# Kernel optimization log

Measured on AMD Instinct MI355X. Metric: run time of the kernel, lower is better.

## Reference

```python
import jax, jax.numpy as jnp
import numpy as np

B, T, D, H = 4096, 128, 32, 64

def _gru_layer(x, W_ih, W_hh, b_ih, b_hh):
    # x: [B, T, in]; W_ih: [3H, in]; W_hh: [3H, H]
    xg = jnp.einsum('bti,gi->btg', x, W_ih) + b_ih  # [B, T, 3H] input gates, one big GEMM
    def step(h, xg_t):
        gh = h @ W_hh.T + b_hh                      # [B, 3H]
        xr, xz, xn = jnp.split(xg_t, 3, axis=-1)
        hr, hz, hn = jnp.split(gh, 3, axis=-1)
        r = jax.nn.sigmoid(xr + hr)
        z = jax.nn.sigmoid(xz + hz)
        n = jnp.tanh(xn + r * hn)
        h_new = (1.0 - z) * n + z * h
        return h_new, h_new
    h0 = jnp.zeros((x.shape[0], W_hh.shape[1]), x.dtype)
    _, hs = jax.lax.scan(step, h0, jnp.swapaxes(xg, 0, 1))  # scan over time
    return jnp.swapaxes(hs, 0, 1)                   # [B, T, H]

def setup_inputs() -> dict:
    key = jax.random.key(0)
    ks = jax.random.split(key, 12)
    s = 0.1
    return {
        'x':     jax.random.normal(ks[0], (B, T, D), jnp.float32),
        'W_ih0': jax.random.normal(ks[1], (3 * H, D), jnp.float32) * s,
        'W_hh0': jax.random.normal(ks[2], (3 * H, H), jnp.float32) * s,
        'b_ih0': jax.random.normal(ks[3], (3 * H,), jnp.float32) * s,
        'b_hh0': jax.random.normal(ks[4], (3 * H,), jnp.float32) * s,
        'W_ih1': jax.random.normal(ks[5], (3 * H, H), jnp.float32) * s,
        'W_hh1': jax.random.normal(ks[6], (3 * H, H), jnp.float32) * s,
        'b_ih1': jax.random.normal(ks[7], (3 * H,), jnp.float32) * s,
        'b_hh1': jax.random.normal(ks[8], (3 * H,), jnp.float32) * s,
        'fc_w':  jax.random.normal(ks[9], (1, H), jnp.float32) * s,
        'fc_b':  jax.random.normal(ks[10], (1,), jnp.float32) * s,
    }

def reference(x, W_ih0, W_hh0, b_ih0, b_hh0, W_ih1, W_hh1, b_ih1, b_hh1, fc_w, fc_b):
    h1 = _gru_layer(x, W_ih0, W_hh0, b_ih0, b_hh0)   # layer 0
    h2 = _gru_layer(h1, W_ih1, W_hh1, b_ih1, b_hh1)  # layer 1
    last = h2[:, -1, :]                              # [B, H]
    out = last @ fc_w.T + fc_b                       # [B, 1]
    return jnp.squeeze(out, axis=-1)                 # [B]
```

## Files before the change

kernel.cpp:

```cpp
#include <hip/hip_runtime.h>

typedef _Float16 f16;
typedef f16 f16x8 __attribute__((ext_vector_type(8)));
typedef f16 f16x4 __attribute__((ext_vector_type(4)));
typedef __fp16 h16x2 __attribute__((ext_vector_type(2)));
typedef float f32x4 __attribute__((ext_vector_type(4)));

#define MFMA16(A, B, C) __builtin_amdgcn_mfma_f32_16x16x32_f16((A), (B), (C), 0, 0, 0)

#define LDS_BARRIER() asm volatile("s_waitcnt lgkmcnt(0)\n\ts_barrier" ::: "memory")

__device__ __forceinline__ f16x8 cvt8(float4 a, float4 b) {
  union { h16x2 h[4]; f16x8 v; } u;
  u.h[0] = __builtin_amdgcn_cvt_pkrtz(a.x, a.y);
  u.h[1] = __builtin_amdgcn_cvt_pkrtz(a.z, a.w);
  u.h[2] = __builtin_amdgcn_cvt_pkrtz(b.x, b.y);
  u.h[3] = __builtin_amdgcn_cvt_pkrtz(b.z, b.w);
  return u.v;
}

__device__ __forceinline__ void gates4(const f32x4& aR, const f32x4& aZ,
                                       const f32x4& aXN, const f32x4& aHN,
                                       float hs[4]) {
#pragma unroll
  for (int r = 0; r < 4; ++r) {
    const float ea = __expf(-aR[r]);
    const float eb = __expf(-aZ[r]);
    const float pa = 1.0f + ea, pb = 1.0f + eb;
    const float inv = __builtin_amdgcn_rcpf(pa * pb);
    const float rg = pb * inv;
    const float zg = pa * inv;
    const float y = aXN[r] + rg * aHN[r];
    const float c = __expf(-2.0f * y);
    const float ng = (1.0f - c) * __builtin_amdgcn_rcpf(1.0f + c);
    hs[r] = ng + zg * (hs[r] - ng);
  }
}

__launch_bounds__(512, 2)
__global__ void gru_fused(const float* __restrict__ x,
                          const float* __restrict__ Wih0, const float* __restrict__ Whh0,
                          const float* __restrict__ bih0, const float* __restrict__ bhh0,
                          const float* __restrict__ Wih1, const float* __restrict__ Whh1,
                          const float* __restrict__ bih1, const float* __restrict__ bhh1,
                          const float* __restrict__ fcw, const float* __restrict__ fcb,
                          float* __restrict__ out) {
  __shared__ f16 H0[2][1024];
  __shared__ f16 H1[2][1024];
  __shared__ float red[4][16];

  const int tid = threadIdx.x;
  const int wave = tid >> 6;
  const int lane = tid & 63;
  const int l15 = lane & 15;
  const int q = lane >> 4;
  const int wa = wave & 3;
  const bool isB = wave >= 4;
  const int b0 = blockIdx.x * 16;

  for (int i = tid; i < 2048; i += 512) {
    ((f16*)H0)[i] = (f16)0.0f;
    ((f16*)H1)[i] = (f16)0.0f;
  }

  f16x8 wAx[3];
  f16x8 wAh[3][2];
  f16x8 wBx[3][2];
  f16x8 wBh[3][2];
  f32x4 bR, bZ, bXN, bHN;
  float fw[4] = {0.f, 0.f, 0.f, 0.f};

  if (!isB) {
#pragma unroll
    for (int g = 0; g < 3; ++g) {
      const int row = g * 64 + 16 * wa + l15;
      const float* p = Wih0 + row * 32 + q * 8;
      wAx[g] = cvt8(*(const float4*)p, *(const float4*)(p + 4));
#pragma unroll
      for (int kf = 0; kf < 2; ++kf) {
        const float* ph = Whh0 + row * 64 + kf * 32 + q * 8;
        wAh[g][kf] = cvt8(*(const float4*)ph, *(const float4*)(ph + 4));
      }
    }
#pragma unroll
    for (int r = 0; r < 4; ++r) {
      const int o = 16 * wa + 4 * q + r;
      bR[r] = bih0[o] + bhh0[o];
      bZ[r] = bih0[64 + o] + bhh0[64 + o];
      bXN[r] = bih0[128 + o];
      bHN[r] = bhh0[128 + o];
    }
  } else {
#pragma unroll
    for (int g = 0; g < 3; ++g) {
      const int row = g * 64 + 16 * wa + l15;
#pragma unroll
      for (int kf = 0; kf < 2; ++kf) {
        const float* p1 = Wih1 + row * 64 + kf * 32 + q * 8;
        wBx[g][kf] = cvt8(*(const float4*)p1, *(const float4*)(p1 + 4));
        const float* p2 = Whh1 + row * 64 + kf * 32 + q * 8;
        wBh[g][kf] = cvt8(*(const float4*)p2, *(const float4*)(p2 + 4));
      }
    }
#pragma unroll
    for (int r = 0; r < 4; ++r) {
      const int o = 16 * wa + 4 * q + r;
      bR[r] = bih1[o] + bhh1[o];
      bZ[r] = bih1[64 + o] + bhh1[64 + o];
      bXN[r] = bih1[128 + o];
      bHN[r] = bhh1[128 + o];
      fw[r] = fcw[o];
    }
  }
  const float fcb0 = fcb[0];

  float hs[4] = {0.f, 0.f, 0.f, 0.f};

  const int wk0 = 16 * wa + 4 * q;
  const int widx = ((wk0 >> 3) * 16 + l15) * 8 + (wk0 & 7);

  auto stepA = [&](const f16* H0r, f16* H0w, float4 xav, float4 xbv) {
    const f16x8 xf = cvt8(xav, xbv);
    const f16x8 h0f0 = *(const f16x8*)&H0r[lane * 8];
    const f16x8 h0f1 = *(const f16x8*)&H0r[512 + lane * 8];
    f32x4 aR = bR, aZ = bZ, aXN = bXN, aHN = bHN;
    aR = MFMA16(wAx[0], xf, aR);
    aZ = MFMA16(wAx[1], xf, aZ);
    aXN = MFMA16(wAx[2], xf, aXN);
    aR = MFMA16(wAh[0][0], h0f0, aR);
    aZ = MFMA16(wAh[1][0], h0f0, aZ);
    aHN = MFMA16(wAh[2][0], h0f0, aHN);
    aR = MFMA16(wAh[0][1], h0f1, aR);
    aZ = MFMA16(wAh[1][1], h0f1, aZ);
    aHN = MFMA16(wAh[2][1], h0f1, aHN);
    gates4(aR, aZ, aXN, aHN, hs);
    union { h16x2 h2[2]; f16x4 v; } uw;
    uw.h2[0] = __builtin_amdgcn_cvt_pkrtz(hs[0], hs[1]);
    uw.h2[1] = __builtin_amdgcn_cvt_pkrtz(hs[2], hs[3]);
    *(f16x4*)&H0w[widx] = uw.v;
  };

  auto stepB = [&](const f16* H0r, const f16* H1r, f16* H1w) {
    const f16x8 g0 = *(const f16x8*)&H0r[lane * 8];
    const f16x8 g1 = *(const f16x8*)&H0r[512 + lane * 8];
    const f16x8 h1f0 = *(const f16x8*)&H1r[lane * 8];
    const f16x8 h1f1 = *(const f16x8*)&H1r[512 + lane * 8];
    f32x4 aR = bR, aZ = bZ, aXN = bXN, aHN = bHN;
    aR = MFMA16(wBx[0][0], g0, aR);
    aZ = MFMA16(wBx[1][0], g0, aZ);
    aXN = MFMA16(wBx[2][0], g0, aXN);
    aR = MFMA16(wBx[0][1], g1, aR);
    aZ = MFMA16(wBx[1][1], g1, aZ);
    aXN = MFMA16(wBx[2][1], g1, aXN);
    aR = MFMA16(wBh[0][0], h1f0, aR);
    aZ = MFMA16(wBh[1][0], h1f0, aZ);
    aHN = MFMA16(wBh[2][0], h1f0, aHN);
    aR = MFMA16(wBh[0][1], h1f1, aR);
    aZ = MFMA16(wBh[1][1], h1f1, aZ);
    aHN = MFMA16(wBh[2][1], h1f1, aHN);
    gates4(aR, aZ, aXN, aHN, hs);
    union { h16x2 h2[2]; f16x4 v; } uw;
    uw.h2[0] = __builtin_amdgcn_cvt_pkrtz(hs[0], hs[1]);
    uw.h2[1] = __builtin_amdgcn_cvt_pkrtz(hs[2], hs[3]);
    *(f16x4*)&H1w[widx] = uw.v;
  };

  __syncthreads();

  const float* xbase = x + (size_t)(b0 + l15) * 4096 + q * 8;
  float4 xa0, xb0, xa1, xb1;
  if (!isB) {
    xa0 = *(const float4*)xbase;
    xb0 = *(const float4*)(xbase + 4);
    xa1 = *(const float4*)(xbase + 32);
    xb1 = *(const float4*)(xbase + 36);
  }

  for (int t = 0; t < 128; t += 2) {
    if (!isB) {
      const float4 cxa = xa0, cxb = xb0;
      if (t + 2 < 128) {
        const float* xp = xbase + (t + 2) * 32;
        xa0 = *(const float4*)xp;
        xb0 = *(const float4*)(xp + 4);
      }
      stepA(H0[0], H0[1], cxa, cxb);
    } else if (t > 0) {
      stepB(H0[0], H1[0], H1[1]);
    }
    LDS_BARRIER();

    if (!isB) {
      const float4 cxa = xa1, cxb = xb1;
      if (t + 3 < 128) {
        const float* xp = xbase + (t + 3) * 32;
        xa1 = *(const float4*)xp;
        xb1 = *(const float4*)(xp + 4);
      }
      stepA(H0[1], H0[0], cxa, cxb);
    } else {
      stepB(H0[1], H1[1], H1[0]);
    }
    LDS_BARRIER();
  }
  if (isB) stepB(H0[0], H1[0], H1[1]);

  if (isB) {
    float partial = fw[0] * hs[0] + fw[1] * hs[1] + fw[2] * hs[2] + fw[3] * hs[3];
    partial += __shfl_down(partial, 16, 64);
    partial += __shfl_down(partial, 32, 64);
    if (lane < 16) red[wa][l15] = partial;
  }
  __syncthreads();
  if (tid < 16) out[b0 + tid] = red[0][tid] + red[1][tid] + red[2][tid] + red[3][tid] + fcb0;
}

extern "C" void kernel_launch(void* const* d_in, const int* in_sizes, int n_in,
                              void* d_out, int out_size, void* d_ws, size_t ws_size,
                              hipStream_t stream) {
  (void)in_sizes; (void)n_in; (void)out_size; (void)d_ws; (void)ws_size;
  const float* x    = (const float*)d_in[0];
  const float* Wih0 = (const float*)d_in[1];
  const float* Whh0 = (const float*)d_in[2];
  const float* bih0 = (const float*)d_in[3];
  const float* bhh0 = (const float*)d_in[4];
  const float* Wih1 = (const float*)d_in[5];
  const float* Whh1 = (const float*)d_in[6];
  const float* bih1 = (const float*)d_in[7];
  const float* bhh1 = (const float*)d_in[8];
  const float* fcw  = (const float*)d_in[9];
  const float* fcb  = (const float*)d_in[10];
  float* out = (float*)d_out;

  gru_fused<<<256, 512, 0, stream>>>(x, Wih0, Whh0, bih0, bhh0,
                                     Wih1, Whh1, bih1, bhh1, fcw, fcb, out);
}
```

Measured before the change: 182.5 us.

## Replace block barriers with LDS flag counters between layer waves

Replaces the per-step block-wide barrier with per-layer LDS counters. Waves spin on the counters and increment them atomically, so layer-0 and layer-1 waves can run up to a few steps apart. H0 becomes a four-deep ring buffer, x is prefetched four steps ahead, and the gate math moves to exp2 in packed pairs with MFMA issue reordered. The aim is to stop the two layers serialising on every barrier. The cost is LDS spin-polling traffic and atomics, and correctness relies on the volatile spin loops plus the LGKM drain.

```diff
diff --git a/kernel.cpp b/kernel.cpp
--- a/kernel.cpp
+++ b/kernel.cpp
@@ -5,10 +5,19 @@
 typedef f16 f16x4 __attribute__((ext_vector_type(4)));
 typedef __fp16 h16x2 __attribute__((ext_vector_type(2)));
 typedef float f32x4 __attribute__((ext_vector_type(4)));
+typedef float f32x2 __attribute__((ext_vector_type(2)));
 
 #define MFMA16(A, B, C) __builtin_amdgcn_mfma_f32_16x16x32_f16((A), (B), (C), 0, 0, 0)
 
-#define LDS_BARRIER() asm volatile("s_waitcnt lgkmcnt(0)\n\ts_barrier" ::: "memory")
+#define LGKM_DRAIN() asm volatile("s_waitcnt lgkmcnt(0)" ::: "memory")
+
+__device__ __forceinline__ float E2(float x) {
+#if __has_builtin(__builtin_amdgcn_exp2f)
+  return __builtin_amdgcn_exp2f(x);
+#else
+  return __expf(x * 0.69314718056f);
+#endif
+}
 
 __device__ __forceinline__ f16x8 cvt8(float4 a, float4 b) {
   union { h16x2 h[4]; f16x8 v; } u;
@@ -19,22 +28,37 @@
   return u.v;
 }
 
-__device__ __forceinline__ void gates4(const f32x4& aR, const f32x4& aZ,
-                                       const f32x4& aXN, const f32x4& aHN,
-                                       float hs[4]) {
-#pragma unroll
-  for (int r = 0; r < 4; ++r) {
-    const float ea = __expf(-aR[r]);
-    const float eb = __expf(-aZ[r]);
-    const float pa = 1.0f + ea, pb = 1.0f + eb;
-    const float inv = __builtin_amdgcn_rcpf(pa * pb);
-    const float rg = pb * inv;
-    const float zg = pa * inv;
-    const float y = aXN[r] + rg * aHN[r];
-    const float c = __expf(-2.0f * y);
-    const float ng = (1.0f - c) * __builtin_amdgcn_rcpf(1.0f + c);
-    hs[r] = ng + zg * (hs[r] - ng);
-  }
+__device__ __forceinline__ void wait2(volatile int* fl, int thrA, int thrB) {
+  while (fl[0] < thrA || fl[1] < thrB) { }
+}
+
+__device__ __forceinline__ void gates_pair(f32x2 aR, f32x2 aZ, f32x2 aXN,
+                                           f32x2 aHN, f32x2& hs) {
+  const float K = -1.44269504f;
+  f32x2 mR = aR * K;
+  f32x2 mZ = aZ * K;
+  f32x2 ea, eb;
+  ea[0] = E2(mR[0]); ea[1] = E2(mR[1]);
+  eb[0] = E2(mZ[0]); eb[1] = E2(mZ[1]);
+  f32x2 pa = ea + 1.0f;
+  f32x2 pb = eb + 1.0f;
+  f32x2 prod = pa * pb;
+  f32x2 inv;
+  inv[0] = __builtin_amdgcn_rcpf(prod[0]);
+  inv[1] = __builtin_amdgcn_rcpf(prod[1]);
+  f32x2 rg = pb * inv;
+  f32x2 zg = pa * inv;
+  f32x2 y = rg * aHN + aXN;
+  f32x2 my = y * (2.0f * K);
+  f32x2 c;
+  c[0] = E2(my[0]); c[1] = E2(my[1]);
+  f32x2 num = 1.0f - c;
+  f32x2 den = 1.0f + c;
+  f32x2 rin;
+  rin[0] = __builtin_amdgcn_rcpf(den[0]);
+  rin[1] = __builtin_amdgcn_rcpf(den[1]);
+  f32x2 ng = num * rin;
+  hs = zg * (hs - ng) + ng;
 }
 
 __launch_bounds__(512, 2)
@@ -45,9 +69,10 @@
                           const float* __restrict__ bih1, const float* __restrict__ bhh1,
                           const float* __restrict__ fcw, const float* __restrict__ fcb,
                           float* __restrict__ out) {
-  __shared__ f16 H0[2][1024];
+  __shared__ f16 H0[4][1024];
   __shared__ f16 H1[2][1024];
   __shared__ float red[4][16];
+  __shared__ int flags[2];
 
   const int tid = threadIdx.x;
   const int wave = tid >> 6;
@@ -58,10 +83,9 @@
   const bool isB = wave >= 4;
   const int b0 = blockIdx.x * 16;
 
-  for (int i = tid; i < 2048; i += 512) {
-    ((f16*)H0)[i] = (f16)0.0f;
-    ((f16*)H1)[i] = (f16)0.0f;
-  }
+  for (int i = tid; i < 4096; i += 512) ((f16*)H0)[i] = (f16)0.0f;
+  for (int i = tid; i < 2048; i += 512) ((f16*)H1)[i] = (f16)0.0f;
+  if (tid == 0) { flags[0] = 0; flags[1] = 0; }
 
   f16x8 wAx[3];
   f16x8 wAh[3][2];
@@ -114,103 +138,105 @@
   }
   const float fcb0 = fcb[0];
 
-  float hs[4] = {0.f, 0.f, 0.f, 0.f};
+  f32x2 hsA = {0.f, 0.f}, hsB2 = {0.f, 0.f};
 
   const int wk0 = 16 * wa + 4 * q;
   const int widx = ((wk0 >> 3) * 16 + l15) * 8 + (wk0 & 7);
 
-  auto stepA = [&](const f16* H0r, f16* H0w, float4 xav, float4 xbv) {
-    const f16x8 xf = cvt8(xav, xbv);
-    const f16x8 h0f0 = *(const f16x8*)&H0r[lane * 8];
-    const f16x8 h0f1 = *(const f16x8*)&H0r[512 + lane * 8];
-    f32x4 aR = bR, aZ = bZ, aXN = bXN, aHN = bHN;
-    aR = MFMA16(wAx[0], xf, aR);
-    aZ = MFMA16(wAx[1], xf, aZ);
-    aXN = MFMA16(wAx[2], xf, aXN);
-    aR = MFMA16(wAh[0][0], h0f0, aR);
-    aZ = MFMA16(wAh[1][0], h0f0, aZ);
-    aHN = MFMA16(wAh[2][0], h0f0, aHN);
-    aR = MFMA16(wAh[0][1], h0f1, aR);
-    aZ = MFMA16(wAh[1][1], h0f1, aZ);
-    aHN = MFMA16(wAh[2][1], h0f1, aHN);
-    gates4(aR, aZ, aXN, aHN, hs);
-    union { h16x2 h2[2]; f16x4 v; } uw;
-    uw.h2[0] = __builtin_amdgcn_cvt_pkrtz(hs[0], hs[1]);
-    uw.h2[1] = __builtin_amdgcn_cvt_pkrtz(hs[2], hs[3]);
-    *(f16x4*)&H0w[widx] = uw.v;
-  };
-
-  auto stepB = [&](const f16* H0r, const f16* H1r, f16* H1w) {
-    const f16x8 g0 = *(const f16x8*)&H0r[lane * 8];
-    const f16x8 g1 = *(const f16x8*)&H0r[512 + lane * 8];
-    const f16x8 h1f0 = *(const f16x8*)&H1r[lane * 8];
-    const f16x8 h1f1 = *(const f16x8*)&H1r[512 + lane * 8];
-    f32x4 aR = bR, aZ = bZ, aXN = bXN, aHN = bHN;
-    aR = MFMA16(wBx[0][0], g0, aR);
-    aZ = MFMA16(wBx[1][0], g0, aZ);
-    aXN = MFMA16(wBx[2][0], g0, aXN);
-    aR = MFMA16(wBx[0][1], g1, aR);
-    aZ = MFMA16(wBx[1][1], g1, aZ);
-    aXN = MFMA16(wBx[2][1], g1, aXN);
-    aR = MFMA16(wBh[0][0], h1f0, aR);
-    aZ = MFMA16(wBh[1][0], h1f0, aZ);
-    aHN = MFMA16(wBh[2][0], h1f0, aHN);
-    aR = MFMA16(wBh[0][1], h1f1, aR);
-    aZ = MFMA16(wBh[1][1], h1f1, aZ);
-    aHN = MFMA16(wBh[2][1], h1f1, aHN);
-    gates4(aR, aZ, aXN, aHN, hs);
-    union { h16x2 h2[2]; f16x4 v; } uw;
-    uw.h2[0] = __builtin_amdgcn_cvt_pkrtz(hs[0], hs[1]);
-    uw.h2[1] = __builtin_amdgcn_cvt_pkrtz(hs[2], hs[3]);
-    *(f16x4*)&H1w[widx] = uw.v;
-  };
-
   __syncthreads();
 
-  const float* xbase = x + (size_t)(b0 + l15) * 4096 + q * 8;
-  float4 xa0, xb0, xa1, xb1;
   if (!isB) {
-    xa0 = *(const float4*)xbase;
-    xb0 = *(const float4*)(xbase + 4);
-    xa1 = *(const float4*)(xbase + 32);
-    xb1 = *(const float4*)(xbase + 36);
-  }
-
-  for (int t = 0; t < 128; t += 2) {
-    if (!isB) {
-      const float4 cxa = xa0, cxb = xb0;
-      if (t + 2 < 128) {
-        const float* xp = xbase + (t + 2) * 32;
-        xa0 = *(const float4*)xp;
-        xb0 = *(const float4*)(xp + 4);
+    const float* xbase = x + (size_t)(b0 + l15) * 4096 + q * 8;
+    float4 xa0 = *(const float4*)(xbase +  0), xb0 = *(const float4*)(xbase +  4);
+    float4 xa1 = *(const float4*)(xbase + 32), xb1 = *(const float4*)(xbase + 36);
+    float4 xa2 = *(const float4*)(xbase + 64), xb2 = *(const float4*)(xbase + 68);
+    float4 xa3 = *(const float4*)(xbase + 96), xb3 = *(const float4*)(xbase + 100);
+
+    auto stepA = [&](int t, const f16* H0r, f16* H0w, float4& pxa, float4& pxb) {
+      wait2(flags, 4 * t, 4 * t - 12);
+      const f16x8 xf = cvt8(pxa, pxb);
+      if (t + 4 < 128) {
+        const float* xp = xbase + (t + 4) * 32;
+        pxa = *(const float4*)xp;
+        pxb = *(const float4*)(xp + 4);
       }
-      stepA(H0[0], H0[1], cxa, cxb);
-    } else if (t > 0) {
-      stepB(H0[0], H1[0], H1[1]);
-    }
-    LDS_BARRIER();
-
-    if (!isB) {
-      const float4 cxa = xa1, cxb = xb1;
-      if (t + 3 < 128) {
-        const float* xp = xbase + (t + 3) * 32;
-        xa1 = *(const float4*)xp;
-        xb1 = *(const float4*)(xp + 4);
-      }
-      stepA(H0[1], H0[0], cxa, cxb);
-    } else {
-      stepB(H0[1], H1[1], H1[0]);
-    }
-    LDS_BARRIER();
-  }
-  if (isB) stepB(H0[0], H1[0], H1[1]);
-
-  if (isB) {
-    float partial = fw[0] * hs[0] + fw[1] * hs[1] + fw[2] * hs[2] + fw[3] * hs[3];
+      const f16x8 h0f0 = *(const f16x8*)&H0r[lane * 8];
+      const f16x8 h0f1 = *(const f16x8*)&H0r[512 + lane * 8];
+      f32x4 aR = bR, aZ = bZ, aXN = bXN, aHN = bHN;
+      aR = MFMA16(wAx[0], xf, aR);
+      aZ = MFMA16(wAx[1], xf, aZ);
+      aR = MFMA16(wAh[0][0], h0f0, aR);
+      aZ = MFMA16(wAh[1][0], h0f0, aZ);
+      aR = MFMA16(wAh[0][1], h0f1, aR);
+      aZ = MFMA16(wAh[1][1], h0f1, aZ);
+      aXN = MFMA16(wAx[2], xf, aXN);
+      aHN = MFMA16(wAh[2][0], h0f0, aHN);
+      aHN = MFMA16(wAh[2][1], h0f1, aHN);
+      gates_pair(f32x2{aR[0], aR[1]}, f32x2{aZ[0], aZ[1]},
+                 f32x2{aXN[0], aXN[1]}, f32x2{aHN[0], aHN[1]}, hsA);
+      gates_pair(f32x2{aR[2], aR[3]}, f32x2{aZ[2], aZ[3]},
+                 f32x2{aXN[2], aXN[3]}, f32x2{aHN[2], aHN[3]}, hsB2);
+      union { h16x2 h2[2]; f16x4 v; } uw;
+      uw.h2[0] = __builtin_amdgcn_cvt_pkrtz(hsA[0], hsA[1]);
+      uw.h2[1] = __builtin_amdgcn_cvt_pkrtz(hsB2[0], hsB2[1]);
+      *(f16x4*)&H0w[widx] = uw.v;
+      LGKM_DRAIN();
+      if (lane == 0) atomicAdd(&flags[0], 1);
+    };
+
+#pragma unroll 1
+    for (int t = 0; t < 128; t += 4) {
+      stepA(t,     &H0[3][0], &H0[0][0], xa0, xb0);
+      stepA(t + 1, &H0[0][0], &H0[1][0], xa1, xb1);
+      stepA(t + 2, &H0[1][0], &H0[2][0], xa2, xb2);
+      stepA(t + 3, &H0[2][0], &H0[3][0], xa3, xb3);
+    }
+  } else {
+    auto stepB = [&](int t, const f16* H0r, const f16* H1r, f16* H1w) {
+      wait2(flags, 4 * t + 4, 4 * t);
+      const f16x8 g0 = *(const f16x8*)&H0r[lane * 8];
+      const f16x8 g1 = *(const f16x8*)&H0r[512 + lane * 8];
+      const f16x8 h1f0 = *(const f16x8*)&H1r[lane * 8];
+      const f16x8 h1f1 = *(const f16x8*)&H1r[512 + lane * 8];
+      f32x4 aR = bR, aZ = bZ, aXN = bXN, aHN = bHN;
+      aR = MFMA16(wBx[0][0], g0, aR);
+      aZ = MFMA16(wBx[1][0], g0, aZ);
+      aR = MFMA16(wBx[0][1], g1, aR);
+      aZ = MFMA16(wBx[1][1], g1, aZ);
+      aR = MFMA16(wBh[0][0], h1f0, aR);
+      aZ = MFMA16(wBh[1][0], h1f0, aZ);
+      aR = MFMA16(wBh[0][1], h1f1, aR);
+      aZ = MFMA16(wBh[1][1], h1f1, aZ);
+      aXN = MFMA16(wBx[2][0], g0, aXN);
+      aXN = MFMA16(wBx[2][1], g1, aXN);
+      aHN = MFMA16(wBh[2][0], h1f0, aHN);
+      aHN = MFMA16(wBh[2][1], h1f1, aHN);
+      gates_pair(f32x2{aR[0], aR[1]}, f32x2{aZ[0], aZ[1]},
+                 f32x2{aXN[0], aXN[1]}, f32x2{aHN[0], aHN[1]}, hsA);
+      gates_pair(f32x2{aR[2], aR[3]}, f32x2{aZ[2], aZ[3]},
+                 f32x2{aXN[2], aXN[3]}, f32x2{aHN[2], aHN[3]}, hsB2);
+      union { h16x2 h2[2]; f16x4 v; } uw;
+      uw.h2[0] = __builtin_amdgcn_cvt_pkrtz(hsA[0], hsA[1]);
+      uw.h2[1] = __builtin_amdgcn_cvt_pkrtz(hsB2[0], hsB2[1]);
+      *(f16x4*)&H1w[widx] = uw.v;
+      LGKM_DRAIN();
+      if (lane == 0) atomicAdd(&flags[1], 1);
+    };
+
+#pragma unroll 1
+    for (int t = 0; t < 128; t += 4) {
+      stepB(t,     &H0[0][0], &H1[1][0], &H1[0][0]);
+      stepB(t + 1, &H0[1][0], &H1[0][0], &H1[1][0]);
+      stepB(t + 2, &H0[2][0], &H1[1][0], &H1[0][0]);
+      stepB(t + 3, &H0[3][0], &H1[0][0], &H1[1][0]);
+    }
+
+    float partial = fw[0] * hsA[0] + fw[1] * hsA[1] + fw[2] * hsB2[0] + fw[3] * hsB2[1];
     partial += __shfl_down(partial, 16, 64);
     partial += __shfl_down(partial, 32, 64);
     if (lane < 16) red[wa][l15] = partial;
   }
+
   __syncthreads();
   if (tid < 16) out[b0 + tid] = red[0][tid] + red[1][tid] + red[2][tid] + red[3][tid] + fcb0;
 }
```

New measurement: 197.9 us. 8.4% more time.
